# Performance work log

Measured on AMD Instinct MI355X. Metric: run time of the kernel, lower is better.

## Reference

```python
import jax, jax.numpy as jnp
import numpy as np

N, E, F_IN, H = 50000, 800000, 16, 128
EPS = 1e-5


def bn(x, gamma, beta):
    # training-mode batchnorm over node dim
    mu = jnp.mean(x, axis=0)
    var = jnp.var(x, axis=0)
    return (x - mu) * jax.lax.rsqrt(var + EPS) * gamma + beta


def gat_conv(x, src, dst, W, att_src, att_dst, bias, heads, out_dim, n):
    h = (x @ W).reshape(n, heads, out_dim)              # [N,H,D]
    a_src = jnp.sum(h * att_src, axis=-1)               # [N,H]
    a_dst = jnp.sum(h * att_dst, axis=-1)               # [N,H]
    e = jax.nn.leaky_relu(a_src[src] + a_dst[dst], 0.2) # [E,H]
    e_max = jax.ops.segment_max(e, dst, num_segments=n)
    e = jnp.exp(e - e_max[dst])
    denom = jax.ops.segment_sum(e, dst, num_segments=n)
    alpha = e / (denom[dst] + 1e-16)                     # [E,H]
    msg = h[src] * alpha[:, :, None]                     # [E,H,D]
    out = jax.ops.segment_sum(msg, dst, num_segments=n)
    return out.reshape(n, heads * out_dim) + bias


def setup_inputs() -> dict:
    key = jax.random.key(0)
    ks = jax.random.split(key, 20)
    s = lambda i, shape, sc=0.05: jax.random.normal(ks[i], shape, jnp.float32) * sc
    inp = {
        "x": jax.random.normal(ks[0], (N, F_IN), jnp.float32),
        "edge_index": jax.random.randint(ks[1], (2, E), 0, N, jnp.int32),
        "W_in": s(2, (F_IN, H)), "b_in": jnp.zeros((H,), jnp.float32),
        "g0": jnp.ones((H,), jnp.float32), "be0": jnp.zeros((H,), jnp.float32),
        "W1": s(3, (H, 2 * H)), "as1": s(4, (2, H)), "ad1": s(5, (2, H)),
        "bias1": jnp.zeros((2 * H,), jnp.float32),
        "g1": jnp.ones((2 * H,), jnp.float32), "be1": jnp.zeros((2 * H,), jnp.float32),
        "W2": s(6, (2 * H, H)), "as2": s(7, (1, H)), "ad2": s(8, (1, H)),
        "bias2": jnp.zeros((H,), jnp.float32),
        "g2": jnp.ones((H,), jnp.float32), "be2": jnp.zeros((H,), jnp.float32),
        "Wf1": s(9, (H, H // 2)), "bf1": jnp.zeros((H // 2,), jnp.float32),
        "gf": jnp.ones((H // 2,), jnp.float32), "bef": jnp.zeros((H // 2,), jnp.float32),
        "Wf2": s(10, (H // 2, 1)), "bf2": jnp.zeros((1,), jnp.float32),
    }
    return inp


def reference(x, edge_index, W_in, b_in, g0, be0, W1, as1, ad1, bias1, g1, be1,
              W2, as2, ad2, bias2, g2, be2, Wf1, bf1, gf, bef, Wf2, bf2):
    n = x.shape[0]
    # PyG GATConv adds self loops by default
    loops = jnp.arange(n, dtype=edge_index.dtype)
    src = jnp.concatenate([edge_index[0], loops])
    dst = jnp.concatenate([edge_index[1], loops])

    h = jax.nn.relu(bn(x @ W_in + b_in, g0, be0))
    h = jax.nn.relu(bn(gat_conv(h, src, dst, W1, as1, ad1, bias1, 2, H, n), g1, be1))
    h = jax.nn.relu(bn(gat_conv(h, src, dst, W2, as2, ad2, bias2, 1, H, n), g2, be2))
    h = jax.nn.relu(bn(h @ Wf1 + bf1, gf, bef))
    # dropout: identity in eval
    return jnp.squeeze(h @ Wf2 + bf2, axis=-1)
```

## Files before the change

kernel.cpp:

```cpp
#include <hip/hip_runtime.h>
#include <hip/hip_bf16.h>


__device__ inline float bf2f(unsigned short u) {
    return __uint_as_float(((unsigned)u) << 16);
}

template<bool BF16OUT>
__global__ __launch_bounds__(256) void gemm_f32(
    const float* __restrict__ A, const float* __restrict__ B,
    const float* __restrict__ bias, void* __restrict__ Cout,
    int M, int Nc, int K)
{
    __shared__ float As[16][68];
    __shared__ float Bs[16][68];
    const int t  = threadIdx.x;
    const int m0 = blockIdx.x * 64;
    const int n0 = blockIdx.y * 64;
    const int tx = t & 15;
    const int ty = t >> 4;
    const int lar = t >> 2;
    const int lac = (t & 3) * 4;
    const int lbr = t >> 4;
    const int lbc = (t & 15) * 4;

    float acc[4][4] = {};
    for (int k0 = 0; k0 < K; k0 += 16) {
        {
            int gr = m0 + lar;
            float4 v = make_float4(0.f, 0.f, 0.f, 0.f);
            if (gr < M) v = *reinterpret_cast<const float4*>(A + (size_t)gr * K + k0 + lac);
            As[lac + 0][lar] = v.x; As[lac + 1][lar] = v.y;
            As[lac + 2][lar] = v.z; As[lac + 3][lar] = v.w;
        }
        {
            float4 v = *reinterpret_cast<const float4*>(B + (size_t)(k0 + lbr) * Nc + n0 + lbc);
            *reinterpret_cast<float4*>(&Bs[lbr][lbc]) = v;
        }
        __syncthreads();
#pragma unroll
        for (int kk = 0; kk < 16; ++kk) {
            float a[4], b[4];
            *reinterpret_cast<float4*>(a) = *reinterpret_cast<const float4*>(&As[kk][ty * 4]);
            *reinterpret_cast<float4*>(b) = *reinterpret_cast<const float4*>(&Bs[kk][tx * 4]);
#pragma unroll
            for (int i = 0; i < 4; ++i)
#pragma unroll
                for (int j = 0; j < 4; ++j)
                    acc[i][j] = fmaf(a[i], b[j], acc[i][j]);
        }
        __syncthreads();
    }
    float bj[4] = {0.f, 0.f, 0.f, 0.f};
    if (bias) *reinterpret_cast<float4*>(bj) = *reinterpret_cast<const float4*>(bias + n0 + tx * 4);
#pragma unroll
    for (int i = 0; i < 4; ++i) {
        int row = m0 + ty * 4 + i;
        if (row < M) {
            float v0 = acc[i][0] + bj[0], v1 = acc[i][1] + bj[1];
            float v2 = acc[i][2] + bj[2], v3 = acc[i][3] + bj[3];
            if constexpr (BF16OUT) {
                __hip_bfloat16 h[4];
                h[0] = __float2bfloat16(v0); h[1] = __float2bfloat16(v1);
                h[2] = __float2bfloat16(v2); h[3] = __float2bfloat16(v3);
                *reinterpret_cast<uint2*>((__hip_bfloat16*)Cout + (size_t)row * Nc + n0 + tx * 4) =
                    *reinterpret_cast<uint2*>(h);
            } else {
                *reinterpret_cast<float4*>((float*)Cout + (size_t)row * Nc + n0 + tx * 4) =
                    make_float4(v0, v1, v2, v3);
            }
        }
    }
}

template<int C>
__global__ __launch_bounds__(256) void bn_stats(const float* __restrict__ y,
                                                double* __restrict__ sums, int Nn)
{
    constexpr int R = (256 / C) < 1 ? 1 : (256 / C);
    const int t = threadIdx.x;
    const int col = (C >= 256) ? t : (t % C);
    const int r0  = (C >= 256) ? 0 : (t / C);
    double s = 0.0, s2 = 0.0;
    for (int row = blockIdx.x * R + r0; row < Nn; row += gridDim.x * R) {
        float v = y[(size_t)row * C + col];
        s += v; s2 += (double)v * (double)v;
    }
    __shared__ double ls[256], ls2[256];
    ls[t] = s; ls2[t] = s2;
    __syncthreads();
    if (t < C) {
#pragma unroll
        for (int k = 1; k < R; ++k) { s += ls[t + k * C]; s2 += ls2[t + k * C]; }
        atomicAdd(&sums[col], s);
        atomicAdd(&sums[C + col], s2);
    }
}

template<int C>
__global__ void bn_fin(const double* __restrict__ sums, const float* __restrict__ g,
                       const float* __restrict__ be, float* __restrict__ sc,
                       float* __restrict__ sh, int Nn)
{
    int c = threadIdx.x;
    if (c < C) {
        double mean = sums[c] / Nn;
        double var  = sums[C + c] / Nn - mean * mean;
        if (var < 0.0) var = 0.0;
        double s = (double)g[c] / sqrt(var + 1e-5);
        sc[c] = (float)s;
        sh[c] = (float)((double)be[c] - mean * s);
    }
}

template<int C>
__global__ __launch_bounds__(256) void bn_apply_relu(float* __restrict__ y,
                                                     const float* __restrict__ sc,
                                                     const float* __restrict__ sh, int total4)
{
    int i = blockIdx.x * blockDim.x + threadIdx.x;
    int stride = gridDim.x * blockDim.x;
    for (; i < total4; i += stride) {
        float4 v = reinterpret_cast<float4*>(y)[i];
        int cb = (i * 4) % C;
        float4 s = *reinterpret_cast<const float4*>(sc + cb);
        float4 h = *reinterpret_cast<const float4*>(sh + cb);
        v.x = fmaxf(fmaf(v.x, s.x, h.x), 0.f);
        v.y = fmaxf(fmaf(v.y, s.y, h.y), 0.f);
        v.z = fmaxf(fmaf(v.z, s.z, h.z), 0.f);
        v.w = fmaxf(fmaf(v.w, s.w, h.w), 0.f);
        reinterpret_cast<float4*>(y)[i] = v;
    }
}

template<int HEADS>
__global__ __launch_bounds__(256) void att_scores(
    const __hip_bfloat16* __restrict__ g, const float* __restrict__ att_s,
    const float* __restrict__ att_d, float* __restrict__ a_s,
    float* __restrict__ a_d, int Nn)
{
    constexpr int C = HEADS * 128;
    constexpr int VEC = C / 64;
    constexpr int GROUP = 128 / VEC;
    int wid  = (blockIdx.x * 256 + threadIdx.x) >> 6;
    int lane = threadIdx.x & 63;
    if (wid >= Nn) return;
    float ps = 0.f, pd = 0.f;
    const __hip_bfloat16* gp = g + (size_t)wid * C + lane * VEC;
    unsigned short u[VEC];
    if constexpr (VEC == 4) *reinterpret_cast<uint2*>(u) = *reinterpret_cast<const uint2*>(gp);
    else                    *reinterpret_cast<unsigned*>(u) = *reinterpret_cast<const unsigned*>(gp);
#pragma unroll
    for (int j = 0; j < VEC; ++j) {
        float v = bf2f(u[j]);
        ps += v * att_s[lane * VEC + j];
        pd += v * att_d[lane * VEC + j];
    }
    for (int off = 1; off < GROUP; off <<= 1) {
        ps += __shfl_xor(ps, off, 64);
        pd += __shfl_xor(pd, off, 64);
    }
    if ((lane & (GROUP - 1)) == 0) {
        int head = (lane * VEC) >> 7;
        a_s[wid * HEADS + head] = ps;
        a_d[wid * HEADS + head] = pd;
    }
}

__global__ void count_edges(const int* __restrict__ ei, int E, int Nn, int* __restrict__ counts)
{
    int k = blockIdx.x * blockDim.x + threadIdx.x;
    if (k >= E + Nn) return;
    int d = (k < E) ? ei[E + k] : (k - E);
    atomicAdd(&counts[d], 1);
}

__global__ void scan_chunk_sum(const int* __restrict__ counts, int Nn, int* __restrict__ csum)
{
    __shared__ int sh[256];
    int i = blockIdx.x * 256 + threadIdx.x;
    sh[threadIdx.x] = (i < Nn) ? counts[i] : 0;
    __syncthreads();
    for (int off = 128; off > 0; off >>= 1) {
        if (threadIdx.x < off) sh[threadIdx.x] += sh[threadIdx.x + off];
        __syncthreads();
    }
    if (threadIdx.x == 0) csum[blockIdx.x] = sh[0];
}

__global__ void scan_chunks(const int* __restrict__ csum, int nchunks, int* __restrict__ coff,
                            int* __restrict__ offsets, int Nn, int Etot)
{
    __shared__ int sh[256];
    int t = threadIdx.x;
    int v = (t < nchunks) ? csum[t] : 0;
    sh[t] = v;
    __syncthreads();
    for (int off = 1; off < 256; off <<= 1) {
        int add = (t >= off) ? sh[t - off] : 0;
        __syncthreads();
        sh[t] += add;
        __syncthreads();
    }
    if (t < nchunks) coff[t] = sh[t] - v;
    if (t == 0) offsets[Nn] = Etot;
}

__global__ void scan_final(const int* __restrict__ counts, int Nn,
                           const int* __restrict__ coff, int* __restrict__ offsets)
{
    __shared__ int sh[256];
    int t = threadIdx.x;
    int i = blockIdx.x * 256 + t;
    int v = (i < Nn) ? counts[i] : 0;
    sh[t] = v;
    __syncthreads();
    for (int off = 1; off < 256; off <<= 1) {
        int add = (t >= off) ? sh[t - off] : 0;
        __syncthreads();
        sh[t] += add;
        __syncthreads();
    }
    if (i < Nn) offsets[i] = coff[blockIdx.x] + sh[t] - v;
}

__global__ void scatter_edges(const int* __restrict__ ei, int E, int Nn,
                              const int* __restrict__ offsets, int* __restrict__ cursor,
                              int* __restrict__ csr_src)
{
    int k = blockIdx.x * blockDim.x + threadIdx.x;
    if (k >= E + Nn) return;
    int s, d;
    if (k < E) { s = ei[k]; d = ei[E + k]; } else { s = k - E; d = k - E; }
    int pos = offsets[d] + atomicAdd(&cursor[d], 1);
    csr_src[pos] = s;
}

template<int C, int HEADS>
__global__ __launch_bounds__(256) void gat_agg_fused(
    const __hip_bfloat16* __restrict__ hfeat,
    const float* __restrict__ a_s, const float* __restrict__ a_d,
    const int* __restrict__ offsets, const int* __restrict__ csr_src,
    const float* __restrict__ bias, float* __restrict__ out, int Nn)
{
    int wid  = (blockIdx.x * 256 + threadIdx.x) >> 6;
    int lane = threadIdx.x & 63;
    if (wid >= Nn) return;
    const int gid = lane >> 4;
    const int gl  = lane & 15;
    const int beg = offsets[wid], end = offsets[wid + 1];

    float ad[HEADS];
#pragma unroll
    for (int h = 0; h < HEADS; ++h) ad[h] = a_d[wid * HEADS + h];

    float m[HEADS];
#pragma unroll
    for (int h = 0; h < HEADS; ++h) m[h] = -1e30f;
    for (int p = beg + lane; p < end; p += 64) {
        int s = csr_src[p];
#pragma unroll
        for (int h = 0; h < HEADS; ++h) {
            float e = a_s[s * HEADS + h] + ad[h];
            e = (e > 0.f) ? e : 0.2f * e;
            m[h] = fmaxf(m[h], e);
        }
    }
    for (int off = 1; off < 64; off <<= 1) {
#pragma unroll
        for (int h = 0; h < HEADS; ++h) m[h] = fmaxf(m[h], __shfl_xor(m[h], off, 64));
    }

    float acc[HEADS][8];
#pragma unroll
    for (int h = 0; h < HEADS; ++h)
#pragma unroll
        for (int j = 0; j < 8; ++j) acc[h][j] = 0.f;
    float wsum[HEADS];
#pragma unroll
    for (int h = 0; h < HEADS; ++h) wsum[h] = 0.f;

    for (int p0 = beg; p0 < end; p0 += 4) {
        int p = p0 + gid;
        bool act = (p < end);
        int s = csr_src[act ? p : beg];
        float w[HEADS];
#pragma unroll
        for (int h = 0; h < HEADS; ++h) {
            float e = a_s[s * HEADS + h] + ad[h];
            e = (e > 0.f) ? e : 0.2f * e;
            w[h] = act ? __expf(e - m[h]) : 0.f;
            wsum[h] += w[h];
        }
        if (act) {
            const __hip_bfloat16* row = hfeat + (size_t)s * C;
#pragma unroll
            for (int h = 0; h < HEADS; ++h) {
                uint4 d = *reinterpret_cast<const uint4*>(row + h * 128 + gl * 8);
                float wh = w[h];
                acc[h][0] = fmaf(wh, bf2f((unsigned short)(d.x & 0xffff)), acc[h][0]);
                acc[h][1] = fmaf(wh, bf2f((unsigned short)(d.x >> 16)),    acc[h][1]);
                acc[h][2] = fmaf(wh, bf2f((unsigned short)(d.y & 0xffff)), acc[h][2]);
                acc[h][3] = fmaf(wh, bf2f((unsigned short)(d.y >> 16)),    acc[h][3]);
                acc[h][4] = fmaf(wh, bf2f((unsigned short)(d.z & 0xffff)), acc[h][4]);
                acc[h][5] = fmaf(wh, bf2f((unsigned short)(d.z >> 16)),    acc[h][5]);
                acc[h][6] = fmaf(wh, bf2f((unsigned short)(d.w & 0xffff)), acc[h][6]);
                acc[h][7] = fmaf(wh, bf2f((unsigned short)(d.w >> 16)),    acc[h][7]);
            }
        }
    }

#pragma unroll
    for (int off = 16; off < 64; off <<= 1) {
#pragma unroll
        for (int h = 0; h < HEADS; ++h) {
            wsum[h] += __shfl_xor(wsum[h], off, 64);
#pragma unroll
            for (int j = 0; j < 8; ++j) acc[h][j] += __shfl_xor(acc[h][j], off, 64);
        }
    }

    if (gid == 0) {
        float* op = out + (size_t)wid * C;
#pragma unroll
        for (int h = 0; h < HEADS; ++h) {
            float inv = 1.f / (wsum[h] + 1e-16f);
            const float* bp = bias + h * 128 + gl * 8;
            float4 v0 = make_float4(
                fmaf(acc[h][0], inv, bp[0]), fmaf(acc[h][1], inv, bp[1]),
                fmaf(acc[h][2], inv, bp[2]), fmaf(acc[h][3], inv, bp[3]));
            float4 v1 = make_float4(
                fmaf(acc[h][4], inv, bp[4]), fmaf(acc[h][5], inv, bp[5]),
                fmaf(acc[h][6], inv, bp[6]), fmaf(acc[h][7], inv, bp[7]));
            *reinterpret_cast<float4*>(op + h * 128 + gl * 8)     = v0;
            *reinterpret_cast<float4*>(op + h * 128 + gl * 8 + 4) = v1;
        }
    }
}

__global__ __launch_bounds__(256) void final_dot(const float* __restrict__ h3,
                                                 const float* __restrict__ w,
                                                 const float* __restrict__ b,
                                                 float* __restrict__ out, int Nn)
{
    int wid  = (blockIdx.x * 256 + threadIdx.x) >> 6;
    int lane = threadIdx.x & 63;
    if (wid >= Nn) return;
    float v = h3[(size_t)wid * 64 + lane] * w[lane];
    for (int off = 32; off > 0; off >>= 1) v += __shfl_xor(v, off, 64);
    if (lane == 0) out[wid] = v + b[0];
}

extern "C" void kernel_launch(void* const* d_in, const int* in_sizes, int n_in,
                              void* d_out, int out_size, void* d_ws, size_t ws_size,
                              hipStream_t stream)
{
    const float* x     = (const float*)d_in[0];
    const int*   ei    = (const int*)d_in[1];
    const float* W_in  = (const float*)d_in[2];
    const float* b_in  = (const float*)d_in[3];
    const float* g0    = (const float*)d_in[4];
    const float* be0   = (const float*)d_in[5];
    const float* W1    = (const float*)d_in[6];
    const float* as1   = (const float*)d_in[7];
    const float* ad1   = (const float*)d_in[8];
    const float* bias1 = (const float*)d_in[9];
    const float* g1    = (const float*)d_in[10];
    const float* be1   = (const float*)d_in[11];
    const float* W2    = (const float*)d_in[12];
    const float* as2   = (const float*)d_in[13];
    const float* ad2   = (const float*)d_in[14];
    const float* bias2 = (const float*)d_in[15];
    const float* g2    = (const float*)d_in[16];
    const float* be2   = (const float*)d_in[17];
    const float* Wf1   = (const float*)d_in[18];
    const float* bf1   = (const float*)d_in[19];
    const float* gf    = (const float*)d_in[20];
    const float* bef   = (const float*)d_in[21];
    const float* Wf2   = (const float*)d_in[22];
    const float* bf2   = (const float*)d_in[23];

    const int N    = in_sizes[0] / 16;
    const int E    = in_sizes[1] / 2;
    const int Etot = E + N;

    char* ws = (char*)d_ws;
    size_t off = 0;
    auto alloc = [&](size_t bytes) {
        size_t o = off;
        off += (bytes + 255) & ~(size_t)255;
        return o;
    };
    float* buf0 = (float*)(ws + alloc((size_t)N * 128 * 4));
    float* buf2 = (float*)(ws + alloc((size_t)N * 256 * 4));
    float* buf1 = (float*)(ws + alloc((size_t)N * 64 * 4));
    __hip_bfloat16* gbuf = (__hip_bfloat16*)(ws + alloc((size_t)N * 256 * 2));
    float* a_s  = (float*)(ws + alloc((size_t)N * 2 * 4));
    float* a_d  = (float*)(ws + alloc((size_t)N * 2 * 4));
    int* offsets  = (int*)(ws + alloc((size_t)(N + 1) * 4));
    int* csr_src  = (int*)(ws + alloc((size_t)Etot * 4));
    int* csum     = (int*)(ws + alloc(256 * 4));
    int* coff     = (int*)(ws + alloc(256 * 4));
    float* scale  = (float*)(ws + alloc(256 * 4));
    float* shift  = (float*)(ws + alloc(256 * 4));
    size_t zone0 = off;
    int* counts      = (int*)(ws + alloc((size_t)N * 4));
    int* cursor      = (int*)(ws + alloc((size_t)N * 4));
    double* sums0    = (double*)(ws + alloc(2 * 128 * 8));
    double* sums1    = (double*)(ws + alloc(2 * 256 * 8));
    double* sums2    = (double*)(ws + alloc(2 * 128 * 8));
    double* sums3    = (double*)(ws + alloc(2 * 64 * 8));
    size_t zone_bytes = off - zone0;

    hipMemsetAsync(ws + zone0, 0, zone_bytes, stream);

    dim3 blk(256);
    const int gM  = (N + 63) / 64;
    const int gE  = (Etot + 255) / 256;
    const int gW  = (N + 3) / 4;
    const int nch = (N + 255) / 256;

    gemm_f32<false><<<dim3(gM, 2), blk, 0, stream>>>(x, W_in, b_in, buf0, N, 128, 16);
    bn_stats<128><<<dim3(400), blk, 0, stream>>>(buf0, sums0, N);
    bn_fin<128><<<1, 128, 0, stream>>>(sums0, g0, be0, scale, shift, N);
    bn_apply_relu<128><<<dim3(2048), blk, 0, stream>>>(buf0, scale, shift, N * 128 / 4);

    count_edges<<<gE, blk, 0, stream>>>(ei, E, N, counts);
    scan_chunk_sum<<<nch, blk, 0, stream>>>(counts, N, csum);
    scan_chunks<<<1, blk, 0, stream>>>(csum, nch, coff, offsets, N, Etot);
    scan_final<<<nch, blk, 0, stream>>>(counts, N, coff, offsets);
    scatter_edges<<<gE, blk, 0, stream>>>(ei, E, N, offsets, cursor, csr_src);

    gemm_f32<true><<<dim3(gM, 4), blk, 0, stream>>>(buf0, W1, nullptr, gbuf, N, 256, 128);
    att_scores<2><<<dim3(gW), blk, 0, stream>>>(gbuf, as1, ad1, a_s, a_d, N);
    gat_agg_fused<256, 2><<<dim3(gW), blk, 0, stream>>>(gbuf, a_s, a_d, offsets, csr_src, bias1, buf2, N);
    bn_stats<256><<<dim3(400), blk, 0, stream>>>(buf2, sums1, N);
    bn_fin<256><<<1, 256, 0, stream>>>(sums1, g1, be1, scale, shift, N);
    bn_apply_relu<256><<<dim3(2048), blk, 0, stream>>>(buf2, scale, shift, N * 256 / 4);

    gemm_f32<true><<<dim3(gM, 2), blk, 0, stream>>>(buf2, W2, nullptr, gbuf, N, 128, 256);
    att_scores<1><<<dim3(gW), blk, 0, stream>>>(gbuf, as2, ad2, a_s, a_d, N);
    gat_agg_fused<128, 1><<<dim3(gW), blk, 0, stream>>>(gbuf, a_s, a_d, offsets, csr_src, bias2, buf0, N);
    bn_stats<128><<<dim3(400), blk, 0, stream>>>(buf0, sums2, N);
    bn_fin<128><<<1, 128, 0, stream>>>(sums2, g2, be2, scale, shift, N);
    bn_apply_relu<128><<<dim3(2048), blk, 0, stream>>>(buf0, scale, shift, N * 128 / 4);

    gemm_f32<false><<<dim3(gM, 1), blk, 0, stream>>>(buf0, Wf1, bf1, buf1, N, 64, 128);
    bn_stats<64><<<dim3(400), blk, 0, stream>>>(buf1, sums3, N);
    bn_fin<64><<<1, 64, 0, stream>>>(sums3, gf, bef, scale, shift, N);
    bn_apply_relu<64><<<dim3(2048), blk, 0, stream>>>(buf1, scale, shift, N * 64 / 4);

    final_dot<<<dim3(gW), blk, 0, stream>>>(buf1, Wf2, bf2, (float*)d_out, N);
}
```

Baseline: 622.5 us.

## Use split-bf16 MFMA GEMMs with fragment-packed BN output for dense layers

Replaces the three large fp32 SIMT GEMMs (W1, W2, Wf1) with MFMA bf16 kernels that use a hi/lo split of operands (three MFMAs per k-step) to approximate fp32 accuracy. The BN-apply+ReLU step now writes activations directly in MFMA fragment layout as hi/lo bf16 pairs, and weights are prepacked each call. This targets the compute cost of the dense projections, in exchange for extra prepack launches and the hi/lo activation write traffic. It is gated on workspace size, with a fallback to the old path.

```diff
diff --git a/kernel.cpp b/kernel.cpp
--- a/kernel.cpp
+++ b/kernel.cpp
@@ -2,8 +2,16 @@
 #include <hip/hip_bf16.h>
 
 
+typedef short bf16x8 __attribute__((ext_vector_type(8)));
+typedef float f32x4  __attribute__((ext_vector_type(4)));
+
 __device__ inline float bf2f(unsigned short u) {
     return __uint_as_float(((unsigned)u) << 16);
+}
+__device__ inline unsigned short f2bf(float f) {
+    union { __hip_bfloat16 h; unsigned short u; } cv;
+    cv.h = __float2bfloat16(f);
+    return cv.u;
 }
 
 template<bool BF16OUT>
@@ -60,10 +68,8 @@
             float v0 = acc[i][0] + bj[0], v1 = acc[i][1] + bj[1];
             float v2 = acc[i][2] + bj[2], v3 = acc[i][3] + bj[3];
             if constexpr (BF16OUT) {
-                __hip_bfloat16 h[4];
-                h[0] = __float2bfloat16(v0); h[1] = __float2bfloat16(v1);
-                h[2] = __float2bfloat16(v2); h[3] = __float2bfloat16(v3);
-                *reinterpret_cast<uint2*>((__hip_bfloat16*)Cout + (size_t)row * Nc + n0 + tx * 4) =
+                unsigned short h[4] = { f2bf(v0), f2bf(v1), f2bf(v2), f2bf(v3) };
+                *reinterpret_cast<uint2*>((unsigned short*)Cout + (size_t)row * Nc + n0 + tx * 4) =
                     *reinterpret_cast<uint2*>(h);
             } else {
                 *reinterpret_cast<float4*>((float*)Cout + (size_t)row * Nc + n0 + tx * 4) =
@@ -71,6 +77,68 @@
             }
         }
     }
+}
+
+template<int KS, bool BF16OUT>
+__global__ __launch_bounds__(256) void mfma_gemm(
+    const bf16x8* __restrict__ ahi, const bf16x8* __restrict__ alo,
+    const bf16x8* __restrict__ bhi, const bf16x8* __restrict__ blo,
+    const float* __restrict__ bias, void* __restrict__ out, int M, int Nc)
+{
+    const int wid  = threadIdx.x >> 6;
+    const int lane = threadIdx.x & 63;
+    const int mt   = blockIdx.x * 4 + wid;
+
+    bf16x8 Ah[KS], Al[KS];
+    size_t abase = (size_t)mt * KS * 64 + lane;
+#pragma unroll
+    for (int ks = 0; ks < KS; ++ks) {
+        Ah[ks] = ahi[abase + ks * 64];
+        Al[ks] = alo[abase + ks * 64];
+    }
+    const int NT    = Nc >> 4;
+    const int colb  = lane & 15;
+    const int rbase = mt * 16 + (lane >> 4) * 4;
+
+    for (int ct = 0; ct < NT; ++ct) {
+        f32x4 acc = {0.f, 0.f, 0.f, 0.f};
+        size_t bbase = (size_t)ct * KS * 64 + lane;
+#pragma unroll
+        for (int ks = 0; ks < KS; ++ks) {
+            bf16x8 Bh = bhi[bbase + ks * 64];
+            bf16x8 Bl = blo[bbase + ks * 64];
+            acc = __builtin_amdgcn_mfma_f32_16x16x32_bf16(Ah[ks], Bh, acc, 0, 0, 0);
+            acc = __builtin_amdgcn_mfma_f32_16x16x32_bf16(Al[ks], Bh, acc, 0, 0, 0);
+            acc = __builtin_amdgcn_mfma_f32_16x16x32_bf16(Ah[ks], Bl, acc, 0, 0, 0);
+        }
+        int col = ct * 16 + colb;
+        float bv = bias ? bias[col] : 0.f;
+#pragma unroll
+        for (int r = 0; r < 4; ++r) {
+            int row = rbase + r;
+            if (row < M) {
+                if constexpr (BF16OUT)
+                    ((unsigned short*)out)[(size_t)row * Nc + col] = f2bf(acc[r] + bv);
+                else
+                    ((float*)out)[(size_t)row * Nc + col] = acc[r] + bv;
+            }
+        }
+    }
+}
+
+__global__ void prepack_b(const float* __restrict__ B, unsigned short* __restrict__ bhi,
+                          unsigned short* __restrict__ blo, int K, int Nc)
+{
+    int idx = blockIdx.x * 256 + threadIdx.x;
+    if (idx >= K * Nc) return;
+    int k = idx / Nc, col = idx - k * Nc;
+    float v = B[idx];
+    unsigned short hi = f2bf(v);
+    unsigned short lo = f2bf(v - bf2f(hi));
+    int KSp = K >> 5;
+    int ct = col >> 4, cin = col & 15, ks = k >> 5, sub = (k >> 3) & 3, j = k & 7;
+    size_t o = (((size_t)(ct * KSp + ks) * 4 + sub) * 16 + cin) * 8 + j;
+    bhi[o] = hi; blo[o] = lo;
 }
 
 template<int C>
@@ -131,6 +199,51 @@
         v.w = fmaxf(fmaf(v.w, s.w, h.w), 0.f);
         reinterpret_cast<float4*>(y)[i] = v;
     }
+}
+
+template<int C>
+__global__ __launch_bounds__(256) void bn_apply_frag(
+    const float* __restrict__ y, const float* __restrict__ sc,
+    const float* __restrict__ sh, uint4* __restrict__ hhi,
+    uint4* __restrict__ hlo, int M, int total )
+{
+    constexpr int G = C / 8;
+    constexpr int KSp = C / 32;
+    int g = blockIdx.x * 256 + threadIdx.x;
+    if (g >= total) return;
+    int row = g / G;
+    int kb  = (g - row * G) * 8;
+    unsigned short hi[8], lo[8];
+    if (row < M) {
+        const float* yp = y + (size_t)row * C + kb;
+        float4 v0 = *reinterpret_cast<const float4*>(yp);
+        float4 v1 = *reinterpret_cast<const float4*>(yp + 4);
+        float4 s0 = *reinterpret_cast<const float4*>(sc + kb);
+        float4 s1 = *reinterpret_cast<const float4*>(sc + kb + 4);
+        float4 h0 = *reinterpret_cast<const float4*>(sh + kb);
+        float4 h1 = *reinterpret_cast<const float4*>(sh + kb + 4);
+        float r[8];
+        r[0] = fmaxf(fmaf(v0.x, s0.x, h0.x), 0.f);
+        r[1] = fmaxf(fmaf(v0.y, s0.y, h0.y), 0.f);
+        r[2] = fmaxf(fmaf(v0.z, s0.z, h0.z), 0.f);
+        r[3] = fmaxf(fmaf(v0.w, s0.w, h0.w), 0.f);
+        r[4] = fmaxf(fmaf(v1.x, s1.x, h1.x), 0.f);
+        r[5] = fmaxf(fmaf(v1.y, s1.y, h1.y), 0.f);
+        r[6] = fmaxf(fmaf(v1.z, s1.z, h1.z), 0.f);
+        r[7] = fmaxf(fmaf(v1.w, s1.w, h1.w), 0.f);
+#pragma unroll
+        for (int j = 0; j < 8; ++j) {
+            hi[j] = f2bf(r[j]);
+            lo[j] = f2bf(r[j] - bf2f(hi[j]));
+        }
+    } else {
+#pragma unroll
+        for (int j = 0; j < 8; ++j) { hi[j] = 0; lo[j] = 0; }
+    }
+    int mt = row >> 4, rin = row & 15, ks = kb >> 5, sub = (kb >> 3) & 3;
+    size_t o = ((size_t)(mt * KSp + ks) * 4 + sub) * 16 + rin;
+    hhi[o] = *reinterpret_cast<uint4*>(hi);
+    hlo[o] = *reinterpret_cast<uint4*>(lo);
 }
 
 template<int HEADS>
@@ -383,6 +496,7 @@
     const int N    = in_sizes[0] / 16;
     const int E    = in_sizes[1] / 2;
     const int Etot = E + N;
+    const int Mpad = ((N + 63) / 64) * 64;
 
     char* ws = (char*)d_ws;
     size_t off = 0;
@@ -411,6 +525,15 @@
     double* sums2    = (double*)(ws + alloc(2 * 128 * 8));
     double* sums3    = (double*)(ws + alloc(2 * 64 * 8));
     size_t zone_bytes = off - zone0;
+    uint4* hhi = (uint4*)(ws + alloc((size_t)Mpad * 256 * 2));
+    uint4* hlo = (uint4*)(ws + alloc((size_t)Mpad * 256 * 2));
+    unsigned short* b1hi = (unsigned short*)(ws + alloc(128 * 256 * 2));
+    unsigned short* b1lo = (unsigned short*)(ws + alloc(128 * 256 * 2));
+    unsigned short* b2hi = (unsigned short*)(ws + alloc(256 * 128 * 2));
+    unsigned short* b2lo = (unsigned short*)(ws + alloc(256 * 128 * 2));
+    unsigned short* bfhi = (unsigned short*)(ws + alloc(128 * 64 * 2));
+    unsigned short* bflo = (unsigned short*)(ws + alloc(128 * 64 * 2));
+    const bool use_mfma = (ws_size >= off);
 
     hipMemsetAsync(ws + zone0, 0, zone_bytes, stream);
 
@@ -419,11 +542,23 @@
     const int gE  = (Etot + 255) / 256;
     const int gW  = (N + 3) / 4;
     const int nch = (N + 255) / 256;
+    const int gMt = Mpad / 64;
+    const int gF128 = (Mpad * 16 + 255) / 256;
+    const int gF256 = (Mpad * 32 + 255) / 256;
+
+    if (use_mfma) {
+        prepack_b<<<dim3((128 * 256 + 255) / 256), blk, 0, stream>>>(W1, b1hi, b1lo, 128, 256);
+        prepack_b<<<dim3((256 * 128 + 255) / 256), blk, 0, stream>>>(W2, b2hi, b2lo, 256, 128);
+        prepack_b<<<dim3((128 * 64 + 255) / 256),  blk, 0, stream>>>(Wf1, bfhi, bflo, 128, 64);
+    }
 
     gemm_f32<false><<<dim3(gM, 2), blk, 0, stream>>>(x, W_in, b_in, buf0, N, 128, 16);
     bn_stats<128><<<dim3(400), blk, 0, stream>>>(buf0, sums0, N);
     bn_fin<128><<<1, 128, 0, stream>>>(sums0, g0, be0, scale, shift, N);
-    bn_apply_relu<128><<<dim3(2048), blk, 0, stream>>>(buf0, scale, shift, N * 128 / 4);
+    if (use_mfma)
+        bn_apply_frag<128><<<dim3(gF128), blk, 0, stream>>>(buf0, scale, shift, hhi, hlo, N, Mpad * 16);
+    else
+        bn_apply_relu<128><<<dim3(2048), blk, 0, stream>>>(buf0, scale, shift, N * 128 / 4);
 
     count_edges<<<gE, blk, 0, stream>>>(ei, E, N, counts);
     scan_chunk_sum<<<nch, blk, 0, stream>>>(counts, N, csum);
@@ -431,21 +566,42 @@
     scan_final<<<nch, blk, 0, stream>>>(counts, N, coff, offsets);
     scatter_edges<<<gE, blk, 0, stream>>>(ei, E, N, offsets, cursor, csr_src);
 
-    gemm_f32<true><<<dim3(gM, 4), blk, 0, stream>>>(buf0, W1, nullptr, gbuf, N, 256, 128);
+    if (use_mfma)
+        mfma_gemm<4, true><<<dim3(gMt), blk, 0, stream>>>(
+            (const bf16x8*)hhi, (const bf16x8*)hlo, (const bf16x8*)b1hi, (const bf16x8*)b1lo,
+            nullptr, gbuf, N, 256);
+    else
+        gemm_f32<true><<<dim3(gM, 4), blk, 0, stream>>>(buf0, W1, nullptr, gbuf, N, 256, 128);
     att_scores<2><<<dim3(gW), blk, 0, stream>>>(gbuf, as1, ad1, a_s, a_d, N);
     gat_agg_fused<256, 2><<<dim3(gW), blk, 0, stream>>>(gbuf, a_s, a_d, offsets, csr_src, bias1, buf2, N);
     bn_stats<256><<<dim3(400), blk, 0, stream>>>(buf2, sums1, N);
     bn_fin<256><<<1, 256, 0, stream>>>(sums1, g1, be1, scale, shift, N);
-    bn_apply_relu<256><<<dim3(2048), blk, 0, stream>>>(buf2, scale, shift, N * 256 / 4);
-
-    gemm_f32<true><<<dim3(gM, 2), blk, 0, stream>>>(buf2, W2, nullptr, gbuf, N, 128, 256);
+    if (use_mfma)
+        bn_apply_frag<256><<<dim3(gF256), blk, 0, stream>>>(buf2, scale, shift, hhi, hlo, N, Mpad * 32);
+    else
+        bn_apply_relu<256><<<dim3(2048), blk, 0, stream>>>(buf2, scale, shift, N * 256 / 4);
+
+    if (use_mfma)
+        mfma_gemm<8, true><<<dim3(gMt), blk, 0, stream>>>(
+            (const bf16x8*)hhi, (const bf16x8*)hlo, (const bf16x8*)b2hi, (const bf16x8*)b2lo,
+            nullptr, gbuf, N, 128);
+    else
+        gemm_f32<true><<<dim3(gM, 2), blk, 0, stream>>>(buf2, W2, nullptr, gbuf, N, 128, 256);
     att_scores<1><<<dim3(gW), blk, 0, stream>>>(gbuf, as2, ad2, a_s, a_d, N);
     gat_agg_fused<128, 1><<<dim3(gW), blk, 0, stream>>>(gbuf, a_s, a_d, offsets, csr_src, bias2, buf0, N);
     bn_stats<128><<<dim3(400), blk, 0, stream>>>(buf0, sums2, N);
     bn_fin<128><<<1, 128, 0, stream>>>(sums2, g2, be2, scale, shift, N);
-    bn_apply_relu<128><<<dim3(2048), blk, 0, stream>>>(buf0, scale, shift, N * 128 / 4);
-
-    gemm_f32<false><<<dim3(gM, 1), blk, 0, stream>>>(buf0, Wf1, bf1, buf1, N, 64, 128);
+    if (use_mfma)
+        bn_apply_frag<128><<<dim3(gF128), blk, 0, stream>>>(buf0, scale, shift, hhi, hlo, N, Mpad * 16);
+    else
+        bn_apply_relu<128><<<dim3(2048), blk, 0, stream>>>(buf0, scale, shift, N * 128 / 4);
+
+    if (use_mfma)
+        mfma_gemm<4, false><<<dim3(gMt), blk, 0, stream>>>(
+            (const bf16x8*)hhi, (const bf16x8*)hlo, (const bf16x8*)bfhi, (const bf16x8*)bflo,
+            bf1, buf1, N, 64);
+    else
+        gemm_f32<false><<<dim3(gM, 1), blk, 0, stream>>>(buf0, Wf1, bf1, buf1, N, 64, 128);
     bn_stats<64><<<dim3(400), blk, 0, stream>>>(buf1, sums3, N);
     bn_fin<64><<<1, 64, 0, stream>>>(sums3, gf, bef, scale, shift, N);
     bn_apply_relu<64><<<dim3(2048), blk, 0, stream>>>(buf1, scale, shift, N * 64 / 4);
```

After: 595.2 us. 1.05x faster.
